# Optimization experiments

Hardware: AMD Instinct MI355X
Metric: run time of the kernel (lower is better)

Reference implementation:

```python
import jax, jax.numpy as jnp
from jax import lax
import numpy as np

I, H, C2 = 14, 64, 2  # input_size, hidden_size, num_classes
B, T = 8192, 256


def _lstm_layer(x_seq, w_ih, w_hh, b_ih, b_hh):
    # x_seq: [T, B, in]; w_ih: [4H, in]; w_hh: [4H, H]; gate order: i, f, g, o (PyTorch)
    Bb = x_seq.shape[1]
    Hh = w_hh.shape[1]
    # precompute input projections for all timesteps in one GEMM
    xg = jnp.einsum('tbi,gi->tbg', x_seq, w_ih) + b_ih + b_hh  # [T, B, 4H]

    def step(carry, xg_t):
        h, c = carry
        g = xg_t + h @ w_hh.T  # [B, 4H]
        i_g, f_g, g_g, o_g = jnp.split(g, 4, axis=-1)
        i_g = jax.nn.sigmoid(i_g)
        f_g = jax.nn.sigmoid(f_g)
        g_g = jnp.tanh(g_g)
        o_g = jax.nn.sigmoid(o_g)
        c = f_g * c + i_g * g_g
        h = o_g * jnp.tanh(c)
        return (h, c), h

    h0 = jnp.zeros((Bb, Hh), x_seq.dtype)
    (_, _), hs = lax.scan(step, (h0, h0), xg)
    return hs  # [T, B, H]


def setup_inputs() -> dict:
    key = jax.random.key(0)
    ks = jax.random.split(key, 13)
    s_ih0 = 1.0 / np.sqrt(H)
    inp = {
        'x': jax.random.normal(ks[0], (B, T, I), dtype=jnp.float32),
        'w_ih0': jax.random.uniform(ks[1], (4 * H, I), jnp.float32, -s_ih0, s_ih0),
        'w_hh0': jax.random.uniform(ks[2], (4 * H, H), jnp.float32, -s_ih0, s_ih0),
        'b_ih0': jax.random.uniform(ks[3], (4 * H,), jnp.float32, -s_ih0, s_ih0),
        'b_hh0': jax.random.uniform(ks[4], (4 * H,), jnp.float32, -s_ih0, s_ih0),
        'w_ih1': jax.random.uniform(ks[5], (4 * H, H), jnp.float32, -s_ih0, s_ih0),
        'w_hh1': jax.random.uniform(ks[6], (4 * H, H), jnp.float32, -s_ih0, s_ih0),
        'b_ih1': jax.random.uniform(ks[7], (4 * H,), jnp.float32, -s_ih0, s_ih0),
        'b_hh1': jax.random.uniform(ks[8], (4 * H,), jnp.float32, -s_ih0, s_ih0),
        'w_fc1': jax.random.uniform(ks[9], (64, H), jnp.float32, -s_ih0, s_ih0),
        'b_fc1': jax.random.uniform(ks[10], (64,), jnp.float32, -s_ih0, s_ih0),
        'w_fc2': jax.random.uniform(ks[11], (C2, 64), jnp.float32, -1.0 / 8, 1.0 / 8),
        'b_fc2': jax.random.uniform(ks[12], (C2,), jnp.float32, -1.0 / 8, 1.0 / 8),
    }
    return inp


def reference(x, w_ih0, w_hh0, b_ih0, b_hh0, w_ih1, w_hh1, b_ih1, b_hh1, w_fc1, b_fc1, w_fc2, b_fc2):
    xt = jnp.transpose(x, (1, 0, 2))  # [T, B, I]
    h1 = _lstm_layer(xt, w_ih0, w_hh0, b_ih0, b_hh0)   # [T, B, H]
    # inter-layer dropout is identity in eval mode
    h2 = _lstm_layer(h1, w_ih1, w_hh1, b_ih1, b_hh1)   # [T, B, H]
    last = h2[-1]                                      # [B, H]
    z = jax.nn.relu(last @ w_fc1.T + b_fc1)            # dropout identity in eval
    return z @ w_fc2.T + b_fc2                         # [B, num_classes]
```

## Files before the change

### kernel.cpp

```cpp
#include <hip/hip_runtime.h>


#define TT 256
#define II 14
#define BB 16
#define NTHREADS 512
#define XP 40
#define HP 72
#define LOG2E 1.44269504088896340736f

typedef _Float16 f16x8 __attribute__((ext_vector_type(8)));
typedef _Float16 f16x4 __attribute__((ext_vector_type(4)));
typedef _Float16 f16x2 __attribute__((ext_vector_type(2)));
typedef float f32x4 __attribute__((ext_vector_type(4)));
typedef float f32x2 __attribute__((ext_vector_type(2)));

__device__ __forceinline__ f32x4 MFMA16(f16x8 a, f16x8 b, f32x4 c) {
  return __builtin_amdgcn_mfma_f32_16x16x32_f16(a, b, c, 0, 0, 0);
}

__device__ __forceinline__ float ex2(float x) {
#if __has_builtin(__builtin_amdgcn_exp2f)
  return __builtin_amdgcn_exp2f(x);
#else
  float r; asm("v_exp_f32 %0, %1" : "=v"(r) : "v"(x)); return r;
#endif
}
__device__ __forceinline__ float rcp_(float x) {
#if __has_builtin(__builtin_amdgcn_rcpf)
  return __builtin_amdgcn_rcpf(x);
#else
  float r; asm("v_rcp_f32 %0, %1" : "=v"(r) : "v"(x)); return r;
#endif
}
__device__ __forceinline__ f16x2 cvt_pk(float a, float b) {
#if __has_builtin(__builtin_amdgcn_cvt_pkrtz)
  return __builtin_bit_cast(f16x2, __builtin_amdgcn_cvt_pkrtz(a, b));
#else
  f16x2 r; r[0] = (_Float16)a; r[1] = (_Float16)b; return r;
#endif
}

__device__ __forceinline__ f16x4 lstm_act(f32x4 si, f32x4 sf, f32x4 sg, f32x4 so,
                                          f32x4& cs) {
  f16x4 hp;
#pragma unroll
  for (int p = 0; p < 2; ++p) {
    f32x2 ui, uf, ug, uo;
    ui.x = ex2(si[2 * p]); ui.y = ex2(si[2 * p + 1]);
    uf.x = ex2(sf[2 * p]); uf.y = ex2(sf[2 * p + 1]);
    ug.x = ex2(sg[2 * p]); ug.y = ex2(sg[2 * p + 1]);
    uo.x = ex2(so[2 * p]); uo.y = ex2(so[2 * p + 1]);
    const f32x2 one = {1.0f, 1.0f};
    const f32x2 fi = ui + one;
    const f32x2 ff = uf + one;
    const f32x2 fg = ug + one;
    const f32x2 pig = fi * fg;
    f32x2 cv; cv.x = cs[2 * p]; cv.y = cs[2 * p + 1];
    const f32x2 num = cv * pig + (ug - one) * ff;
    const f32x2 den = pig * ff;
    f32x2 rd; rd.x = rcp_(den.x); rd.y = rcp_(den.y);
    const f32x2 c = num * rd;
    cs[2 * p] = c.x; cs[2 * p + 1] = c.y;
    const f32x2 ctl = c * (f32x2){2.0f * LOG2E, 2.0f * LOG2E};
    f32x2 ut; ut.x = ex2(ctl.x); ut.y = ex2(ctl.y);
    const f32x2 dh = (uo + one) * (ut + one);
    f32x2 rh; rh.x = rcp_(dh.x); rh.y = rcp_(dh.y);
    const f32x2 h = (ut - one) * rh;
    const f16x2 h2 = cvt_pk(h.x, h.y);
    hp[2 * p] = h2[0];
    hp[2 * p + 1] = h2[1];
  }
  return hp;
}

__global__ void __launch_bounds__(NTHREADS, 4) fused_lstm(
    const float* __restrict__ x,
    const float* __restrict__ w_ih0, const float* __restrict__ w_hh0,
    const float* __restrict__ b_ih0, const float* __restrict__ b_hh0,
    const float* __restrict__ w_ih1, const float* __restrict__ w_hh1,
    const float* __restrict__ b_ih1, const float* __restrict__ b_hh1,
    const float* __restrict__ w_fc1, const float* __restrict__ b_fc1,
    const float* __restrict__ w_fc2, const float* __restrict__ b_fc2,
    float* __restrict__ out) {
  __shared__ char smem[11776];

  const int tid = threadIdx.x;
  const int wv = tid >> 6;
  const int grp = wv >> 2;
  const int wl = wv & 3;
  const int l = tid & 63;
  const int row16 = l & 15;
  const int kblk = l >> 4;

  const int b0 = blockIdx.x * BB;

  f16x8 wIn[4][2], wRec[4][2];
  f32x4 bias[4];
#pragma unroll
  for (int gt = 0; gt < 4; ++gt) {
    const float sc = (gt == 2) ? (2.0f * LOG2E) : (-LOG2E);
    const int g = gt * 64 + wl * 16 + row16;
    if (grp == 0) {
      f16x8 v;
#pragma unroll
      for (int j = 0; j < 8; ++j) {
        const int k = kblk * 8 + j;
        v[j] = (k < II) ? (_Float16)(w_ih0[g * II + k] * sc) : (_Float16)0.0f;
      }
      wIn[gt][0] = v;
#pragma unroll
      for (int ks = 0; ks < 2; ++ks) {
        const int ko = ks * 32 + kblk * 8;
        f16x8 vr;
#pragma unroll
        for (int j = 0; j < 8; ++j) vr[j] = (_Float16)(w_hh0[g * 64 + ko + j] * sc);
        wRec[gt][ks] = vr;
      }
    } else {
#pragma unroll
      for (int ks = 0; ks < 2; ++ks) {
        const int ko = ks * 32 + kblk * 8;
        f16x8 vi, vr;
#pragma unroll
        for (int j = 0; j < 8; ++j) vi[j] = (_Float16)(w_ih1[g * 64 + ko + j] * sc);
#pragma unroll
        for (int j = 0; j < 8; ++j) vr[j] = (_Float16)(w_hh1[g * 64 + ko + j] * sc);
        wIn[gt][ks] = vi;
        wRec[gt][ks] = vr;
      }
    }
    const int gb = gt * 64 + wl * 16 + kblk * 4;
#pragma unroll
    for (int r = 0; r < 4; ++r) {
      bias[gt][r] = (grp == 0) ? (b_ih0[gb + r] + b_hh0[gb + r]) * sc
                               : (b_ih1[gb + r] + b_hh1[gb + r]) * sc;
    }
  }

  for (int i = tid; i < 11776 / 4; i += NTHREADS) ((int*)smem)[i] = 0;

  const int n0 = tid / II, k0 = tid - n0 * II;
  const bool hasx = tid < BB * II;
  const float* xp0 = x + (size_t)(b0 + (hasx ? n0 : 0)) * (TT * II) + k0;

  _Float16* H1 = (_Float16*)smem;
  _Float16* H0 = (_Float16*)(smem + 4608);
  _Float16* XS = (_Float16*)(smem + 9216);

  __syncthreads();
  if (hasx) XS[n0 * XP + k0] = (_Float16)xp0[0];
  __syncthreads();

  f32x4 cs = {0.f, 0.f, 0.f, 0.f};

  const int boff = row16 * HP + kblk * 8;
  const int woff = row16 * HP + wl * 16 + kblk * 4;

  if (grp == 0) {
    f32x4 acc[4];
#pragma unroll
    for (int gt = 0; gt < 4; ++gt) acc[gt] = bias[gt];
    const f16x8 bx = *(const f16x8*)(XS + row16 * XP + kblk * 8);
    const f16x8 bhA = *(const f16x8*)(H0 + 1152 + boff);
    const f16x8 bhB = *(const f16x8*)(H0 + 1152 + 32 + boff);
    __builtin_amdgcn_s_setprio(1);
#pragma unroll
    for (int gt = 0; gt < 4; ++gt) {
      acc[gt] = MFMA16(wIn[gt][0], bx, acc[gt]);
      acc[gt] = MFMA16(wRec[gt][0], bhA, acc[gt]);
      acc[gt] = MFMA16(wRec[gt][1], bhB, acc[gt]);
    }
    __builtin_amdgcn_s_setprio(0);
    const float xn = hasx ? (float)xp0[II] : 0.0f;
    const f16x4 hp = lstm_act(acc[0], acc[1], acc[2], acc[3], cs);
    *(f16x4*)(H0 + woff) = hp;
    if (hasx) XS[640 + n0 * XP + k0] = (_Float16)xn;
  }
  __syncthreads();

#pragma unroll 2
  for (int t = 1; t < TT; ++t) {
    const int pc = t & 1, pp = pc ^ 1;
    if (grp == 0) {
      f32x4 acc[4];
#pragma unroll
      for (int gt = 0; gt < 4; ++gt) acc[gt] = bias[gt];
      const f16x8 bx = *(const f16x8*)(XS + pc * 640 + row16 * XP + kblk * 8);
      const f16x8 bhA = *(const f16x8*)(H0 + pp * 1152 + boff);
      const f16x8 bhB = *(const f16x8*)(H0 + pp * 1152 + 32 + boff);
      __builtin_amdgcn_s_setprio(1);
#pragma unroll
      for (int gt = 0; gt < 4; ++gt) {
        acc[gt] = MFMA16(wIn[gt][0], bx, acc[gt]);
        acc[gt] = MFMA16(wRec[gt][0], bhA, acc[gt]);
        acc[gt] = MFMA16(wRec[gt][1], bhB, acc[gt]);
      }
      __builtin_amdgcn_s_setprio(0);
      const int tn = (t + 1 < TT) ? (t + 1) : (TT - 1);
      const float xn = hasx ? xp0[(size_t)tn * II] : 0.0f;
      const f16x4 hp = lstm_act(acc[0], acc[1], acc[2], acc[3], cs);
      *(f16x4*)(H0 + pc * 1152 + woff) = hp;
      if (hasx) XS[pp * 640 + n0 * XP + k0] = (_Float16)xn;
    } else {
      f32x4 acc[4];
#pragma unroll
      for (int gt = 0; gt < 4; ++gt) acc[gt] = bias[gt];
      const f16x8 bgA = *(const f16x8*)(H0 + pp * 1152 + boff);
      const f16x8 bgB = *(const f16x8*)(H0 + pp * 1152 + 32 + boff);
      const f16x8 bhA = *(const f16x8*)(H1 + pc * 1152 + boff);
      const f16x8 bhB = *(const f16x8*)(H1 + pc * 1152 + 32 + boff);
      __builtin_amdgcn_s_setprio(1);
#pragma unroll
      for (int gt = 0; gt < 4; ++gt) {
        acc[gt] = MFMA16(wIn[gt][0], bgA, acc[gt]);
        acc[gt] = MFMA16(wIn[gt][1], bgB, acc[gt]);
        acc[gt] = MFMA16(wRec[gt][0], bhA, acc[gt]);
        acc[gt] = MFMA16(wRec[gt][1], bhB, acc[gt]);
      }
      __builtin_amdgcn_s_setprio(0);
      const f16x4 hp = lstm_act(acc[0], acc[1], acc[2], acc[3], cs);
      *(f16x4*)(H1 + pp * 1152 + woff) = hp;
    }
    __syncthreads();
  }

  if (grp == 1) {
    f32x4 acc[4];
#pragma unroll
    for (int gt = 0; gt < 4; ++gt) acc[gt] = bias[gt];
    const f16x8 bgA = *(const f16x8*)(H0 + 1152 + boff);
    const f16x8 bgB = *(const f16x8*)(H0 + 1152 + 32 + boff);
    const f16x8 bhA = *(const f16x8*)(H1 + boff);
    const f16x8 bhB = *(const f16x8*)(H1 + 32 + boff);
    __builtin_amdgcn_s_setprio(1);
#pragma unroll
    for (int gt = 0; gt < 4; ++gt) {
      acc[gt] = MFMA16(wIn[gt][0], bgA, acc[gt]);
      acc[gt] = MFMA16(wIn[gt][1], bgB, acc[gt]);
      acc[gt] = MFMA16(wRec[gt][0], bhA, acc[gt]);
      acc[gt] = MFMA16(wRec[gt][1], bhB, acc[gt]);
    }
    __builtin_amdgcn_s_setprio(0);
    const f16x4 hp = lstm_act(acc[0], acc[1], acc[2], acc[3], cs);
    *(f16x4*)(H1 + 1152 + woff) = hp;
  }
  __syncthreads();

  const _Float16* h1f = (const _Float16*)(smem + 2304);
  float* zbuf = (float*)(smem + 4608);
  {
    float4 w1r[16];
#pragma unroll
    for (int k4 = 0; k4 < 16; ++k4)
      w1r[k4] = *(const float4*)(w_fc1 + l * 64 + k4 * 4);
    const float b1l = b_fc1[l];
#pragma unroll
    for (int bi = 0; bi < 2; ++bi) {
      const int n = wv * 2 + bi;
      float s = b1l;
#pragma unroll
      for (int k4 = 0; k4 < 16; ++k4) {
        const float4 wq = w1r[k4];
        s = fmaf((float)h1f[n * HP + k4 * 4 + 0], wq.x, s);
        s = fmaf((float)h1f[n * HP + k4 * 4 + 1], wq.y, s);
        s = fmaf((float)h1f[n * HP + k4 * 4 + 2], wq.z, s);
        s = fmaf((float)h1f[n * HP + k4 * 4 + 3], wq.w, s);
      }
      zbuf[n * 64 + l] = fmaxf(s, 0.0f);
    }
  }
  __syncthreads();
  if (tid < 2 * BB) {
    const int n = tid >> 1, cc = tid & 1;
    float s = b_fc2[cc];
    for (int j = 0; j < 64; ++j) s = fmaf(w_fc2[cc * 64 + j], zbuf[n * 64 + j], s);
    out[(size_t)(b0 + n) * 2 + cc] = s;
  }
}

extern "C" void kernel_launch(void* const* d_in, const int* in_sizes, int n_in,
                              void* d_out, int out_size, void* d_ws, size_t ws_size,
                              hipStream_t stream) {
  (void)in_sizes; (void)n_in; (void)d_ws; (void)ws_size; (void)out_size;
  const float* x = (const float*)d_in[0];
  const float* w_ih0 = (const float*)d_in[1];
  const float* w_hh0 = (const float*)d_in[2];
  const float* b_ih0 = (const float*)d_in[3];
  const float* b_hh0 = (const float*)d_in[4];
  const float* w_ih1 = (const float*)d_in[5];
  const float* w_hh1 = (const float*)d_in[6];
  const float* b_ih1 = (const float*)d_in[7];
  const float* b_hh1 = (const float*)d_in[8];
  const float* w_fc1 = (const float*)d_in[9];
  const float* b_fc1 = (const float*)d_in[10];
  const float* w_fc2 = (const float*)d_in[11];
  const float* b_fc2 = (const float*)d_in[12];

  fused_lstm<<<dim3(8192 / BB), dim3(NTHREADS), 0, stream>>>(
      x, w_ih0, w_hh0, b_ih0, b_hh0, w_ih1, w_hh1, b_ih1, b_hh1,
      w_fc1, b_fc1, w_fc2, b_fc2, (float*)d_out);
}
```

Before: 317.8 us.

## Process two 16-sample batch tiles per wave to double ILP per recurrence step

Doubles the batch slice per block from 16 to 32 samples. Each wave now runs two independent MFMA/activation chains (tiles A and B) that share the same register-resident weights, and the shared-memory buffers grow to hold both tiles. This halves the block count and the barriers per sample, and gives each wave more independent work to hide MFMA and transcendental latency in the serial timestep loop. In exchange it uses more registers and LDS (launch bounds lowered to 2 blocks/SM), and with half as many blocks some CUs may be left with less parallelism.

```diff
diff --git a/kernel.cpp b/kernel.cpp
--- a/kernel.cpp
+++ b/kernel.cpp
@@ -3,10 +3,12 @@
 
 #define TT 256
 #define II 14
-#define BB 16
+#define BB 32
 #define NTHREADS 512
 #define XP 40
 #define HP 72
+#define HSTR 2304
+#define XSTR 1280
 #define LOG2E 1.44269504088896340736f
 
 typedef _Float16 f16x8 __attribute__((ext_vector_type(8)));
@@ -74,7 +76,7 @@
   return hp;
 }
 
-__global__ void __launch_bounds__(NTHREADS, 4) fused_lstm(
+__global__ void __launch_bounds__(NTHREADS, 2) fused_lstm(
     const float* __restrict__ x,
     const float* __restrict__ w_ih0, const float* __restrict__ w_hh0,
     const float* __restrict__ b_ih0, const float* __restrict__ b_hh0,
@@ -83,7 +85,10 @@
     const float* __restrict__ w_fc1, const float* __restrict__ b_fc1,
     const float* __restrict__ w_fc2, const float* __restrict__ b_fc2,
     float* __restrict__ out) {
-  __shared__ char smem[11776];
+  __shared__ char smem[23552];
+  _Float16* H1 = (_Float16*)smem;
+  _Float16* H0 = (_Float16*)(smem + 9216);
+  _Float16* XS = (_Float16*)(smem + 18432);
 
   const int tid = threadIdx.x;
   const int wv = tid >> 6;
@@ -138,117 +143,155 @@
     }
   }
 
-  for (int i = tid; i < 11776 / 4; i += NTHREADS) ((int*)smem)[i] = 0;
+  for (int i = tid; i < 23552 / 4; i += NTHREADS) ((int*)smem)[i] = 0;
 
   const int n0 = tid / II, k0 = tid - n0 * II;
   const bool hasx = tid < BB * II;
   const float* xp0 = x + (size_t)(b0 + (hasx ? n0 : 0)) * (TT * II) + k0;
 
-  _Float16* H1 = (_Float16*)smem;
-  _Float16* H0 = (_Float16*)(smem + 4608);
-  _Float16* XS = (_Float16*)(smem + 9216);
-
   __syncthreads();
   if (hasx) XS[n0 * XP + k0] = (_Float16)xp0[0];
   __syncthreads();
 
-  f32x4 cs = {0.f, 0.f, 0.f, 0.f};
-
-  const int boff = row16 * HP + kblk * 8;
-  const int woff = row16 * HP + wl * 16 + kblk * 4;
-
-  if (grp == 0) {
-    f32x4 acc[4];
-#pragma unroll
-    for (int gt = 0; gt < 4; ++gt) acc[gt] = bias[gt];
-    const f16x8 bx = *(const f16x8*)(XS + row16 * XP + kblk * 8);
-    const f16x8 bhA = *(const f16x8*)(H0 + 1152 + boff);
-    const f16x8 bhB = *(const f16x8*)(H0 + 1152 + 32 + boff);
-    __builtin_amdgcn_s_setprio(1);
-#pragma unroll
-    for (int gt = 0; gt < 4; ++gt) {
-      acc[gt] = MFMA16(wIn[gt][0], bx, acc[gt]);
-      acc[gt] = MFMA16(wRec[gt][0], bhA, acc[gt]);
-      acc[gt] = MFMA16(wRec[gt][1], bhB, acc[gt]);
-    }
-    __builtin_amdgcn_s_setprio(0);
-    const float xn = hasx ? (float)xp0[II] : 0.0f;
-    const f16x4 hp = lstm_act(acc[0], acc[1], acc[2], acc[3], cs);
-    *(f16x4*)(H0 + woff) = hp;
-    if (hasx) XS[640 + n0 * XP + k0] = (_Float16)xn;
+  f32x4 cs0 = {0.f, 0.f, 0.f, 0.f}, cs1 = {0.f, 0.f, 0.f, 0.f};
+
+  const int boffA = row16 * HP + kblk * 8;
+  const int boffB = (16 + row16) * HP + kblk * 8;
+  const int woffA = row16 * HP + wl * 16 + kblk * 4;
+  const int woffB = (16 + row16) * HP + wl * 16 + kblk * 4;
+
+  {
+    const float xn = hasx ? xp0[II] : 0.0f;
+    if (grp == 0) {
+      f32x4 accA[4], accB[4];
+#pragma unroll
+      for (int gt = 0; gt < 4; ++gt) { accA[gt] = bias[gt]; accB[gt] = bias[gt]; }
+      const f16x8 bxA = *(const f16x8*)(XS + row16 * XP + kblk * 8);
+      const f16x8 bxB = *(const f16x8*)(XS + (16 + row16) * XP + kblk * 8);
+      __builtin_amdgcn_s_setprio(1);
+#pragma unroll
+      for (int gt = 0; gt < 4; ++gt) {
+        accA[gt] = MFMA16(wIn[gt][0], bxA, accA[gt]);
+        accB[gt] = MFMA16(wIn[gt][0], bxB, accB[gt]);
+      }
+      __builtin_amdgcn_s_setprio(0);
+      const f16x4 hA = lstm_act(accA[0], accA[1], accA[2], accA[3], cs0);
+      const f16x4 hB = lstm_act(accB[0], accB[1], accB[2], accB[3], cs1);
+      *(f16x4*)(H0 + woffA) = hA;
+      *(f16x4*)(H0 + woffB) = hB;
+    }
+    if (hasx) XS[XSTR + n0 * XP + k0] = (_Float16)xn;
   }
   __syncthreads();
 
 #pragma unroll 2
   for (int t = 1; t < TT; ++t) {
     const int pc = t & 1, pp = pc ^ 1;
+    const int tn = (t + 1 < TT) ? (t + 1) : (TT - 1);
+    const float xn = hasx ? xp0[(size_t)tn * II] : 0.0f;
+
     if (grp == 0) {
-      f32x4 acc[4];
-#pragma unroll
-      for (int gt = 0; gt < 4; ++gt) acc[gt] = bias[gt];
-      const f16x8 bx = *(const f16x8*)(XS + pc * 640 + row16 * XP + kblk * 8);
-      const f16x8 bhA = *(const f16x8*)(H0 + pp * 1152 + boff);
-      const f16x8 bhB = *(const f16x8*)(H0 + pp * 1152 + 32 + boff);
+      f32x4 accA[4], accB[4];
+#pragma unroll
+      for (int gt = 0; gt < 4; ++gt) { accA[gt] = bias[gt]; accB[gt] = bias[gt]; }
+      const _Float16* xsb = XS + pc * XSTR;
+      const _Float16* h0r = H0 + pp * HSTR;
+      const f16x8 bxA = *(const f16x8*)(xsb + row16 * XP + kblk * 8);
+      const f16x8 bxB = *(const f16x8*)(xsb + (16 + row16) * XP + kblk * 8);
+      const f16x8 bhA0 = *(const f16x8*)(h0r + boffA);
+      const f16x8 bhA1 = *(const f16x8*)(h0r + 32 + boffA);
+      const f16x8 bhB0 = *(const f16x8*)(h0r + boffB);
+      const f16x8 bhB1 = *(const f16x8*)(h0r + 32 + boffB);
       __builtin_amdgcn_s_setprio(1);
 #pragma unroll
       for (int gt = 0; gt < 4; ++gt) {
-        acc[gt] = MFMA16(wIn[gt][0], bx, acc[gt]);
-        acc[gt] = MFMA16(wRec[gt][0], bhA, acc[gt]);
-        acc[gt] = MFMA16(wRec[gt][1], bhB, acc[gt]);
+        accA[gt] = MFMA16(wIn[gt][0], bxA, accA[gt]);
+        accB[gt] = MFMA16(wIn[gt][0], bxB, accB[gt]);
+        accA[gt] = MFMA16(wRec[gt][0], bhA0, accA[gt]);
+        accB[gt] = MFMA16(wRec[gt][0], bhB0, accB[gt]);
+        accA[gt] = MFMA16(wRec[gt][1], bhA1, accA[gt]);
+        accB[gt] = MFMA16(wRec[gt][1], bhB1, accB[gt]);
       }
       __builtin_amdgcn_s_setprio(0);
-      const int tn = (t + 1 < TT) ? (t + 1) : (TT - 1);
-      const float xn = hasx ? xp0[(size_t)tn * II] : 0.0f;
-      const f16x4 hp = lstm_act(acc[0], acc[1], acc[2], acc[3], cs);
-      *(f16x4*)(H0 + pc * 1152 + woff) = hp;
-      if (hasx) XS[pp * 640 + n0 * XP + k0] = (_Float16)xn;
+      const f16x4 hA = lstm_act(accA[0], accA[1], accA[2], accA[3], cs0);
+      const f16x4 hB = lstm_act(accB[0], accB[1], accB[2], accB[3], cs1);
+      _Float16* h0w = H0 + pc * HSTR;
+      *(f16x4*)(h0w + woffA) = hA;
+      *(f16x4*)(h0w + woffB) = hB;
     } else {
-      f32x4 acc[4];
-#pragma unroll
-      for (int gt = 0; gt < 4; ++gt) acc[gt] = bias[gt];
-      const f16x8 bgA = *(const f16x8*)(H0 + pp * 1152 + boff);
-      const f16x8 bgB = *(const f16x8*)(H0 + pp * 1152 + 32 + boff);
-      const f16x8 bhA = *(const f16x8*)(H1 + pc * 1152 + boff);
-      const f16x8 bhB = *(const f16x8*)(H1 + pc * 1152 + 32 + boff);
+      f32x4 accA[4], accB[4];
+#pragma unroll
+      for (int gt = 0; gt < 4; ++gt) { accA[gt] = bias[gt]; accB[gt] = bias[gt]; }
+      const _Float16* h0r = H0 + pp * HSTR;
+      const _Float16* h1r = H1 + pc * HSTR;
+      const f16x8 bgA0 = *(const f16x8*)(h0r + boffA);
+      const f16x8 bgA1 = *(const f16x8*)(h0r + 32 + boffA);
+      const f16x8 bgB0 = *(const f16x8*)(h0r + boffB);
+      const f16x8 bgB1 = *(const f16x8*)(h0r + 32 + boffB);
+      const f16x8 bhA0 = *(const f16x8*)(h1r + boffA);
+      const f16x8 bhA1 = *(const f16x8*)(h1r + 32 + boffA);
+      const f16x8 bhB0 = *(const f16x8*)(h1r + boffB);
+      const f16x8 bhB1 = *(const f16x8*)(h1r + 32 + boffB);
       __builtin_amdgcn_s_setprio(1);
 #pragma unroll
       for (int gt = 0; gt < 4; ++gt) {
-        acc[gt] = MFMA16(wIn[gt][0], bgA, acc[gt]);
-        acc[gt] = MFMA16(wIn[gt][1], bgB, acc[gt]);
-        acc[gt] = MFMA16(wRec[gt][0], bhA, acc[gt]);
-        acc[gt] = MFMA16(wRec[gt][1], bhB, acc[gt]);
+        accA[gt] = MFMA16(wIn[gt][0], bgA0, accA[gt]);
+        accB[gt] = MFMA16(wIn[gt][0], bgB0, accB[gt]);
+        accA[gt] = MFMA16(wIn[gt][1], bgA1, accA[gt]);
+        accB[gt] = MFMA16(wIn[gt][1], bgB1, accB[gt]);
+        accA[gt] = MFMA16(wRec[gt][0], bhA0, accA[gt]);
+        accB[gt] = MFMA16(wRec[gt][0], bhB0, accB[gt]);
+        accA[gt] = MFMA16(wRec[gt][1], bhA1, accA[gt]);
+        accB[gt] = MFMA16(wRec[gt][1], bhB1, accB[gt]);
       }
       __builtin_amdgcn_s_setprio(0);
-      const f16x4 hp = lstm_act(acc[0], acc[1], acc[2], acc[3], cs);
-      *(f16x4*)(H1 + pp * 1152 + woff) = hp;
-    }
+      const f16x4 hA = lstm_act(accA[0], accA[1], accA[2], accA[3], cs0);
+      const f16x4 hB = lstm_act(accB[0], accB[1], accB[2], accB[3], cs1);
+      _Float16* h1w = H1 + pp * HSTR;
+      *(f16x4*)(h1w + woffA) = hA;
+      *(f16x4*)(h1w + woffB) = hB;
+    }
+    if (hasx) XS[pp * XSTR + n0 * XP + k0] = (_Float16)xn;
     __syncthreads();
   }
 
   if (grp == 1) {
-    f32x4 acc[4];
-#pragma unroll
-    for (int gt = 0; gt < 4; ++gt) acc[gt] = bias[gt];
-    const f16x8 bgA = *(const f16x8*)(H0 + 1152 + boff);
-    const f16x8 bgB = *(const f16x8*)(H0 + 1152 + 32 + boff);
-    const f16x8 bhA = *(const f16x8*)(H1 + boff);
-    const f16x8 bhB = *(const f16x8*)(H1 + 32 + boff);
+    f32x4 accA[4], accB[4];
+#pragma unroll
+    for (int gt = 0; gt < 4; ++gt) { accA[gt] = bias[gt]; accB[gt] = bias[gt]; }
+    const _Float16* h0r = H0 + HSTR;
+    const _Float16* h1r = H1;
+    const f16x8 bgA0 = *(const f16x8*)(h0r + boffA);
+    const f16x8 bgA1 = *(const f16x8*)(h0r + 32 + boffA);
+    const f16x8 bgB0 = *(const f16x8*)(h0r + boffB);
+    const f16x8 bgB1 = *(const f16x8*)(h0r + 32 + boffB);
+    const f16x8 bhA0 = *(const f16x8*)(h1r + boffA);
+    const f16x8 bhA1 = *(const f16x8*)(h1r + 32 + boffA);
+    const f16x8 bhB0 = *(const f16x8*)(h1r + boffB);
+    const f16x8 bhB1 = *(const f16x8*)(h1r + 32 + boffB);
     __builtin_amdgcn_s_setprio(1);
 #pragma unroll
     for (int gt = 0; gt < 4; ++gt) {
-      acc[gt] = MFMA16(wIn[gt][0], bgA, acc[gt]);
-      acc[gt] = MFMA16(wIn[gt][1], bgB, acc[gt]);
-      acc[gt] = MFMA16(wRec[gt][0], bhA, acc[gt]);
-      acc[gt] = MFMA16(wRec[gt][1], bhB, acc[gt]);
+      accA[gt] = MFMA16(wIn[gt][0], bgA0, accA[gt]);
+      accB[gt] = MFMA16(wIn[gt][0], bgB0, accB[gt]);
+      accA[gt] = MFMA16(wIn[gt][1], bgA1, accA[gt]);
+      accB[gt] = MFMA16(wIn[gt][1], bgB1, accB[gt]);
+      accA[gt] = MFMA16(wRec[gt][0], bhA0, accA[gt]);
+      accB[gt] = MFMA16(wRec[gt][0], bhB0, accB[gt]);
+      accA[gt] = MFMA16(wRec[gt][1], bhA1, accA[gt]);
+      accB[gt] = MFMA16(wRec[gt][1], bhB1, accB[gt]);
     }
     __builtin_amdgcn_s_setprio(0);
-    const f16x4 hp = lstm_act(acc[0], acc[1], acc[2], acc[3], cs);
-    *(f16x4*)(H1 + 1152 + woff) = hp;
-  }
-  __syncthreads();
-
-  const _Float16* h1f = (const _Float16*)(smem + 2304);
-  float* zbuf = (float*)(smem + 4608);
+    const f16x4 hA = lstm_act(accA[0], accA[1], accA[2], accA[3], cs0);
+    const f16x4 hB = lstm_act(accB[0], accB[1], accB[2], accB[3], cs1);
+    _Float16* h1w = H1 + HSTR;
+    *(f16x4*)(h1w + woffA) = hA;
+    *(f16x4*)(h1w + woffB) = hB;
+  }
+  __syncthreads();
+
+  const _Float16* h1f = H1 + HSTR;
+  float* zbuf = (float*)(smem + 9216);
   {
     float4 w1r[16];
 #pragma unroll
@@ -256,8 +299,8 @@
       w1r[k4] = *(const float4*)(w_fc1 + l * 64 + k4 * 4);
     const float b1l = b_fc1[l];
 #pragma unroll
-    for (int bi = 0; bi < 2; ++bi) {
-      const int n = wv * 2 + bi;
+    for (int bi = 0; bi < 4; ++bi) {
+      const int n = wv * 4 + bi;
       float s = b1l;
 #pragma unroll
       for (int k4 = 0; k4 < 16; ++k4) {
```

Result: slower. 359.4 us (+13.1%).

## Precompute next step's input projection after activation to shorten recurrent critical path

Applied to the files above, without the earlier changes.

Splits each LSTM step's MFMAs so that only the recurrent h@W_hh products remain on the serial path. The input-projection MFMAs for the following step (x for layer 0, h0 for layer 1) run after the activation, into a second accumulator set. This adds a third x staging buffer and a deeper software pipeline with ping-pong accumulators. The cost is more registers, extra shared memory, and more complex prologue and epilogue handling that could contain indexing errors.

```diff
diff --git a/kernel.cpp b/kernel.cpp
--- a/kernel.cpp
+++ b/kernel.cpp
@@ -7,6 +7,8 @@
 #define NTHREADS 512
 #define XP 40
 #define HP 72
+#define HSTR 1152
+#define XSTR 640
 #define LOG2E 1.44269504088896340736f
 
 typedef _Float16 f16x8 __attribute__((ext_vector_type(8)));
@@ -83,7 +85,10 @@
     const float* __restrict__ w_fc1, const float* __restrict__ b_fc1,
     const float* __restrict__ w_fc2, const float* __restrict__ b_fc2,
     float* __restrict__ out) {
-  __shared__ char smem[11776];
+  __shared__ char smem[13056];
+  _Float16* H1 = (_Float16*)smem;
+  _Float16* H0 = (_Float16*)(smem + 4608);
+  _Float16* XS = (_Float16*)(smem + 9216);
 
   const int tid = threadIdx.x;
   const int wv = tid >> 6;
@@ -92,7 +97,6 @@
   const int l = tid & 63;
   const int row16 = l & 15;
   const int kblk = l >> 4;
-
   const int b0 = blockIdx.x * BB;
 
   f16x8 wIn[4][2], wRec[4][2];
@@ -109,6 +113,7 @@
         v[j] = (k < II) ? (_Float16)(w_ih0[g * II + k] * sc) : (_Float16)0.0f;
       }
       wIn[gt][0] = v;
+      wIn[gt][1] = v;
 #pragma unroll
       for (int ks = 0; ks < 2; ++ks) {
         const int ko = ks * 32 + kblk * 8;
@@ -138,112 +143,122 @@
     }
   }
 
-  for (int i = tid; i < 11776 / 4; i += NTHREADS) ((int*)smem)[i] = 0;
+  for (int i = tid; i < 13056 / 4; i += NTHREADS) ((int*)smem)[i] = 0;
 
   const int n0 = tid / II, k0 = tid - n0 * II;
   const bool hasx = tid < BB * II;
   const float* xp0 = x + (size_t)(b0 + (hasx ? n0 : 0)) * (TT * II) + k0;
 
-  _Float16* H1 = (_Float16*)smem;
-  _Float16* H0 = (_Float16*)(smem + 4608);
-  _Float16* XS = (_Float16*)(smem + 9216);
-
-  __syncthreads();
-  if (hasx) XS[n0 * XP + k0] = (_Float16)xp0[0];
+  __syncthreads();
+  if (hasx) {
+    XS[n0 * XP + k0] = (_Float16)xp0[0];
+    XS[XSTR + n0 * XP + k0] = (_Float16)xp0[II];
+  }
   __syncthreads();
 
   f32x4 cs = {0.f, 0.f, 0.f, 0.f};
-
   const int boff = row16 * HP + kblk * 8;
   const int woff = row16 * HP + wl * 16 + kblk * 4;
 
+  f32x4 accA[4], accB[4];
+
   if (grp == 0) {
-    f32x4 acc[4];
-#pragma unroll
-    for (int gt = 0; gt < 4; ++gt) acc[gt] = bias[gt];
-    const f16x8 bx = *(const f16x8*)(XS + row16 * XP + kblk * 8);
-    const f16x8 bhA = *(const f16x8*)(H0 + 1152 + boff);
-    const f16x8 bhB = *(const f16x8*)(H0 + 1152 + 32 + boff);
-    __builtin_amdgcn_s_setprio(1);
+    const f16x8 bx0 = *(const f16x8*)(XS + row16 * XP + kblk * 8);
+#pragma unroll
+    for (int gt = 0; gt < 4; ++gt) accB[gt] = MFMA16(wIn[gt][0], bx0, bias[gt]);
+    const f16x4 hp = lstm_act(accB[0], accB[1], accB[2], accB[3], cs);
+    *(f16x4*)(H0 + woff) = hp;
+    const f16x8 bx1 = *(const f16x8*)(XS + XSTR + row16 * XP + kblk * 8);
+#pragma unroll
+    for (int gt = 0; gt < 4; ++gt) accA[gt] = MFMA16(wIn[gt][0], bx1, bias[gt]);
+  } else {
+#pragma unroll
+    for (int gt = 0; gt < 4; ++gt) { accA[gt] = bias[gt]; accB[gt] = bias[gt]; }
+  }
+  if (hasx) XS[2 * XSTR + n0 * XP + k0] = (_Float16)xp0[2 * II];
+  __syncthreads();
+
+  int hpub = HSTR, hrd = 0;
+  int xsA = XSTR, xsB = 2 * XSTR, xsC = 0;
+
+  auto step = [&](int t, f32x4(&accC)[4], f32x4(&accN)[4]) {
+    const int tn = (t + 2 < TT) ? (t + 2) : (TT - 1);
+    const float xn = hasx ? xp0[(size_t)tn * II] : 0.0f;
+    if (grp == 0) {
+      const f16x8 bhA = *(const f16x8*)(H0 + hrd + boff);
+      const f16x8 bhB = *(const f16x8*)(H0 + hrd + 32 + boff);
+      __builtin_amdgcn_s_setprio(1);
+#pragma unroll
+      for (int gt = 0; gt < 4; ++gt) {
+        accC[gt] = MFMA16(wRec[gt][0], bhA, accC[gt]);
+        accC[gt] = MFMA16(wRec[gt][1], bhB, accC[gt]);
+      }
+      __builtin_amdgcn_s_setprio(0);
+      const f16x4 hp = lstm_act(accC[0], accC[1], accC[2], accC[3], cs);
+      *(f16x4*)(H0 + hpub + woff) = hp;
+      const f16x8 bx = *(const f16x8*)(XS + xsB + row16 * XP + kblk * 8);
+#pragma unroll
+      for (int gt = 0; gt < 4; ++gt) accN[gt] = MFMA16(wIn[gt][0], bx, bias[gt]);
+    } else {
+      const f16x8 bhA = *(const f16x8*)(H1 + hrd + boff);
+      const f16x8 bhB = *(const f16x8*)(H1 + hrd + 32 + boff);
+      __builtin_amdgcn_s_setprio(1);
+#pragma unroll
+      for (int gt = 0; gt < 4; ++gt) {
+        accC[gt] = MFMA16(wRec[gt][0], bhA, accC[gt]);
+        accC[gt] = MFMA16(wRec[gt][1], bhB, accC[gt]);
+      }
+      __builtin_amdgcn_s_setprio(0);
+      if (t >= 2) {
+        const f16x4 hp = lstm_act(accC[0], accC[1], accC[2], accC[3], cs);
+        *(f16x4*)(H1 + hpub + woff) = hp;
+      }
+      const f16x8 bgA = *(const f16x8*)(H0 + hrd + boff);
+      const f16x8 bgB = *(const f16x8*)(H0 + hrd + 32 + boff);
+#pragma unroll
+      for (int gt = 0; gt < 4; ++gt) {
+        accN[gt] = MFMA16(wIn[gt][0], bgA, bias[gt]);
+        accN[gt] = MFMA16(wIn[gt][1], bgB, accN[gt]);
+      }
+    }
+    if (hasx) XS[xsC + n0 * XP + k0] = (_Float16)xn;
+    __syncthreads();
+    int tmp = hpub; hpub = hrd; hrd = tmp;
+    int tA = xsA; xsA = xsB; xsB = xsC; xsC = tA;
+  };
+
+  for (int t = 1; t < TT - 1; t += 2) {
+    step(t, accA, accB);
+    step(t + 1, accB, accA);
+  }
+  step(TT - 1, accA, accB);
+
+  if (grp == 1) {
+    const f16x8 bhA = *(const f16x8*)(H1 + HSTR + boff);
+    const f16x8 bhB = *(const f16x8*)(H1 + HSTR + 32 + boff);
 #pragma unroll
     for (int gt = 0; gt < 4; ++gt) {
-      acc[gt] = MFMA16(wIn[gt][0], bx, acc[gt]);
-      acc[gt] = MFMA16(wRec[gt][0], bhA, acc[gt]);
-      acc[gt] = MFMA16(wRec[gt][1], bhB, acc[gt]);
-    }
-    __builtin_amdgcn_s_setprio(0);
-    const float xn = hasx ? (float)xp0[II] : 0.0f;
-    const f16x4 hp = lstm_act(acc[0], acc[1], acc[2], acc[3], cs);
-    *(f16x4*)(H0 + woff) = hp;
-    if (hasx) XS[640 + n0 * XP + k0] = (_Float16)xn;
-  }
-  __syncthreads();
-
-#pragma unroll 2
-  for (int t = 1; t < TT; ++t) {
-    const int pc = t & 1, pp = pc ^ 1;
-    if (grp == 0) {
-      f32x4 acc[4];
-#pragma unroll
-      for (int gt = 0; gt < 4; ++gt) acc[gt] = bias[gt];
-      const f16x8 bx = *(const f16x8*)(XS + pc * 640 + row16 * XP + kblk * 8);
-      const f16x8 bhA = *(const f16x8*)(H0 + pp * 1152 + boff);
-      const f16x8 bhB = *(const f16x8*)(H0 + pp * 1152 + 32 + boff);
-      __builtin_amdgcn_s_setprio(1);
-#pragma unroll
-      for (int gt = 0; gt < 4; ++gt) {
-        acc[gt] = MFMA16(wIn[gt][0], bx, acc[gt]);
-        acc[gt] = MFMA16(wRec[gt][0], bhA, acc[gt]);
-        acc[gt] = MFMA16(wRec[gt][1], bhB, acc[gt]);
-      }
-      __builtin_amdgcn_s_setprio(0);
-      const int tn = (t + 1 < TT) ? (t + 1) : (TT - 1);
-      const float xn = hasx ? xp0[(size_t)tn * II] : 0.0f;
-      const f16x4 hp = lstm_act(acc[0], acc[1], acc[2], acc[3], cs);
-      *(f16x4*)(H0 + pc * 1152 + woff) = hp;
-      if (hasx) XS[pp * 640 + n0 * XP + k0] = (_Float16)xn;
-    } else {
-      f32x4 acc[4];
-#pragma unroll
-      for (int gt = 0; gt < 4; ++gt) acc[gt] = bias[gt];
-      const f16x8 bgA = *(const f16x8*)(H0 + pp * 1152 + boff);
-      const f16x8 bgB = *(const f16x8*)(H0 + pp * 1152 + 32 + boff);
-      const f16x8 bhA = *(const f16x8*)(H1 + pc * 1152 + boff);
-      const f16x8 bhB = *(const f16x8*)(H1 + pc * 1152 + 32 + boff);
-      __builtin_amdgcn_s_setprio(1);
-#pragma unroll
-      for (int gt = 0; gt < 4; ++gt) {
-        acc[gt] = MFMA16(wIn[gt][0], bgA, acc[gt]);
-        acc[gt] = MFMA16(wIn[gt][1], bgB, acc[gt]);
-        acc[gt] = MFMA16(wRec[gt][0], bhA, acc[gt]);
-        acc[gt] = MFMA16(wRec[gt][1], bhB, acc[gt]);
-      }
-      __builtin_amdgcn_s_setprio(0);
-      const f16x4 hp = lstm_act(acc[0], acc[1], acc[2], acc[3], cs);
-      *(f16x4*)(H1 + pp * 1152 + woff) = hp;
-    }
-    __syncthreads();
-  }
-
+      accB[gt] = MFMA16(wRec[gt][0], bhA, accB[gt]);
+      accB[gt] = MFMA16(wRec[gt][1], bhB, accB[gt]);
+    }
+    const f16x4 hp = lstm_act(accB[0], accB[1], accB[2], accB[3], cs);
+    *(f16x4*)(H1 + woff) = hp;
+  }
+  __syncthreads();
   if (grp == 1) {
-    f32x4 acc[4];
-#pragma unroll
-    for (int gt = 0; gt < 4; ++gt) acc[gt] = bias[gt];
-    const f16x8 bgA = *(const f16x8*)(H0 + 1152 + boff);
-    const f16x8 bgB = *(const f16x8*)(H0 + 1152 + 32 + boff);
+    const f16x8 bgA = *(const f16x8*)(H0 + HSTR + boff);
+    const f16x8 bgB = *(const f16x8*)(H0 + HSTR + 32 + boff);
     const f16x8 bhA = *(const f16x8*)(H1 + boff);
     const f16x8 bhB = *(const f16x8*)(H1 + 32 + boff);
-    __builtin_amdgcn_s_setprio(1);
 #pragma unroll
     for (int gt = 0; gt < 4; ++gt) {
-      acc[gt] = MFMA16(wIn[gt][0], bgA, acc[gt]);
-      acc[gt] = MFMA16(wIn[gt][1], bgB, acc[gt]);
-      acc[gt] = MFMA16(wRec[gt][0], bhA, acc[gt]);
-      acc[gt] = MFMA16(wRec[gt][1], bhB, acc[gt]);
-    }
-    __builtin_amdgcn_s_setprio(0);
-    const f16x4 hp = lstm_act(acc[0], acc[1], acc[2], acc[3], cs);
-    *(f16x4*)(H1 + 1152 + woff) = hp;
+      accA[gt] = MFMA16(wIn[gt][0], bgA, bias[gt]);
+      accA[gt] = MFMA16(wIn[gt][1], bgB, accA[gt]);
+      accA[gt] = MFMA16(wRec[gt][0], bhA, accA[gt]);
+      accA[gt] = MFMA16(wRec[gt][1], bhB, accA[gt]);
+    }
+    const f16x4 hp = lstm_act(accA[0], accA[1], accA[2], accA[3], cs);
+    *(f16x4*)(H1 + HSTR + woff) = hp;
   }
   __syncthreads();
 
```

Result: slower. 324.5 us (+2.1%).
